# Kernel tuning notes

Measured on AMD Instinct MI355X. Metric: run time of the kernel, lower is better.

## Reference

```python
import jax, jax.numpy as jnp
import numpy as np

D_MODEL, D_K, D_V, H = 1024, 64, 64, 16
LN_EPS = 1e-5


def setup_inputs() -> dict:
    key = jax.random.key(0)
    ks = jax.random.split(key, 16)
    B, NQ, NK = 2, 1024, 1024
    queries = jax.random.normal(ks[0], (B, NQ, D_MODEL), dtype=jnp.float32)
    keys = jax.random.normal(ks[1], (B, NK, D_MODEL), dtype=jnp.float32)
    values = jax.random.normal(ks[2], (B, NK, D_MODEL), dtype=jnp.float32)
    attention_mask = jax.random.randint(ks[3], (B, H, NQ, NK), 0, 2).astype(jnp.bool_)
    attention_weights = jax.random.uniform(ks[4], (B, H, NQ, NK), dtype=jnp.float32)
    # Linear params, stored (in, out) so x @ W + b
    def xavier(k, shape):
        lim = float(np.sqrt(6.0 / (shape[0] + shape[1])))
        return jax.random.uniform(k, shape, jnp.float32, -lim, lim)
    Wq = xavier(ks[5], (D_MODEL, H * D_K)); bq = jnp.zeros((H * D_K,), jnp.float32)
    Wk = xavier(ks[6], (D_MODEL, H * D_K)); bk = jnp.zeros((H * D_K,), jnp.float32)
    Wv = xavier(ks[7], (D_MODEL, H * D_V)); bv = jnp.zeros((H * D_V,), jnp.float32)
    Wo = xavier(ks[8], (H * D_V, D_MODEL)); bo = jnp.zeros((D_MODEL,), jnp.float32)
    gamma = jnp.ones((D_MODEL,), jnp.float32)
    beta = jnp.zeros((D_MODEL,), jnp.float32)
    return dict(queries=queries, keys=keys, values=values,
                attention_mask=attention_mask, attention_weights=attention_weights,
                Wq=Wq, bq=bq, Wk=Wk, bk=bk, Wv=Wv, bv=bv, Wo=Wo, bo=bo,
                gamma=gamma, beta=beta)


def layer_norm(x, gamma, beta):
    mu = jnp.mean(x, axis=-1, keepdims=True)
    var = jnp.mean(jnp.square(x - mu), axis=-1, keepdims=True)
    return (x - mu) * jax.lax.rsqrt(var + LN_EPS) * gamma + beta


def reference(queries, keys, values, attention_mask, attention_weights,
              Wq, bq, Wk, bk, Wv, bv, Wo, bo, gamma, beta):
    B, NQ, _ = queries.shape
    NK = keys.shape[1]
    q = (queries @ Wq + bq).reshape(B, NQ, H, D_K).transpose(0, 2, 1, 3)  # b h nq dk
    k = (keys @ Wk + bk).reshape(B, NK, H, D_K).transpose(0, 2, 1, 3)    # b h nk dk
    v = (values @ Wv + bv).reshape(B, NK, H, D_V).transpose(0, 2, 1, 3)  # b h nk dv
    att = jnp.einsum('bhqd,bhkd->bhqk', q, k) / jnp.sqrt(jnp.float32(D_K))
    att = att * attention_weights
    att = jnp.where(attention_mask, -jnp.inf, att)
    att = jax.nn.softmax(att, axis=-1)  # dropout is identity in eval
    out = jnp.einsum('bhqk,bhkd->bhqd', att, v)
    out = out.transpose(0, 2, 1, 3).reshape(B, NQ, H * D_V)
    out = out @ Wo + bo
    # post-LN residual (identity_map_reordering=False)
    return layer_norm(queries + out, gamma, beta)
```

## Files before the change

kernel.cpp:

```cpp
#include <hip/hip_runtime.h>
#include <hip/hip_bf16.h>
#include <math.h>

#define B_   2
#define H_   16
#define NSEQ 1024
#define DM   1024
#define DKV  64
#define LNEPS 1e-5f

typedef __attribute__((ext_vector_type(8))) short s16x8;
typedef __attribute__((ext_vector_type(4))) float f32x4;
typedef __attribute__((ext_vector_type(4))) unsigned u32x4;

__device__ inline short f2bf(float f) {
    __hip_bfloat16 h = __float2bfloat16(f);
    return *reinterpret_cast<short*>(&h);
}

__global__ void detect_mask(const unsigned* __restrict__ mask_words, int* __restrict__ flag) {
    unsigned f = 0;
    for (int i = 0; i < 256; ++i) f |= (mask_words[i] > 1u) ? 1u : 0u;
    *flag = (int)f;
}

__global__ __launch_bounds__(256) void cast_bf16(const float* __restrict__ in,
                                                 short* __restrict__ out, int n) {
    int i = (blockIdx.x * 256 + threadIdx.x) * 8;
    if (i >= n) return;
    f32x4 a = *(const f32x4*)(in + i);
    f32x4 b = *(const f32x4*)(in + i + 4);
    s16x8 o;
    o[0]=f2bf(a[0]); o[1]=f2bf(a[1]); o[2]=f2bf(a[2]); o[3]=f2bf(a[3]);
    o[4]=f2bf(b[0]); o[5]=f2bf(b[1]); o[6]=f2bf(b[2]); o[7]=f2bf(b[3]);
    *(s16x8*)(out + i) = o;
}

__global__ __launch_bounds__(256) void castT_bf16(const float* __restrict__ W,
                                                  short* __restrict__ Wt) {
    __shared__ float tl[32][33];
    const int k0 = blockIdx.y * 32, n0 = blockIdx.x * 32;
    const int r = threadIdx.x >> 3, c4 = (threadIdx.x & 7) * 4;
    *(float4*)&tl[r][c4] = *(const float4*)(W + (size_t)(k0 + r) * DM + n0 + c4);
    __syncthreads();
    unsigned u0 = (unsigned short)f2bf(tl[c4+0][r]) | ((unsigned)(unsigned short)f2bf(tl[c4+1][r]) << 16);
    unsigned u1 = (unsigned short)f2bf(tl[c4+2][r]) | ((unsigned)(unsigned short)f2bf(tl[c4+3][r]) << 16);
    uint2 pk; pk.x = u0; pk.y = u1;
    *(uint2*)(Wt + (size_t)(n0 + r) * DM + k0 + c4) = pk;
}

__global__ __launch_bounds__(256) void gemm_bf16(
    const short* __restrict__ A, const short* __restrict__ Wt,
    const float* __restrict__ bias, const float* __restrict__ resid,
    void* __restrict__ outp, int mode)
{
    const int t  = threadIdx.x;
    const int wv = t >> 6, l = t & 63, lg = l >> 4, li = l & 15;
    const int wr = wv >> 1, wc = wv & 1;
    const int c0 = blockIdx.x * 64, m0 = blockIdx.y * 64;

    __shared__ short Asl[64 * 64];
    __shared__ short Bsl[64 * 64];

    f32x4 acc[2][2] = {};

    const int sr = t >> 2, scol = (t & 3) * 16;
    const int sw = (sr & 7) << 3;

    s16x8 a0 = *(const s16x8*)(A  + (size_t)(m0 + sr) * DM + scol);
    s16x8 a1 = *(const s16x8*)(A  + (size_t)(m0 + sr) * DM + scol + 8);
    s16x8 b0 = *(const s16x8*)(Wt + (size_t)(c0 + sr) * DM + scol);
    s16x8 b1 = *(const s16x8*)(Wt + (size_t)(c0 + sr) * DM + scol + 8);

    for (int k0 = 0; k0 < DM; k0 += 64) {
        __syncthreads();
        *(s16x8*)&Asl[sr * 64 + (scol ^ sw)]       = a0;
        *(s16x8*)&Asl[sr * 64 + ((scol + 8) ^ sw)] = a1;
        *(s16x8*)&Bsl[sr * 64 + (scol ^ sw)]       = b0;
        *(s16x8*)&Bsl[sr * 64 + ((scol + 8) ^ sw)] = b1;
        __syncthreads();
        if (k0 + 64 < DM) {
            a0 = *(const s16x8*)(A  + (size_t)(m0 + sr) * DM + k0 + 64 + scol);
            a1 = *(const s16x8*)(A  + (size_t)(m0 + sr) * DM + k0 + 64 + scol + 8);
            b0 = *(const s16x8*)(Wt + (size_t)(c0 + sr) * DM + k0 + 64 + scol);
            b1 = *(const s16x8*)(Wt + (size_t)(c0 + sr) * DM + k0 + 64 + scol + 8);
        }
        #pragma unroll
        for (int kh = 0; kh < 2; ++kh) {
            s16x8 af[2], bf[2];
            #pragma unroll
            for (int fi = 0; fi < 2; ++fi) {
                const int row = wr * 32 + fi * 16 + li;
                af[fi] = *(const s16x8*)&Asl[row * 64 + ((kh * 32 + lg * 8) ^ ((row & 7) << 3))];
            }
            #pragma unroll
            for (int fj = 0; fj < 2; ++fj) {
                const int row = wc * 32 + fj * 16 + li;
                bf[fj] = *(const s16x8*)&Bsl[row * 64 + ((kh * 32 + lg * 8) ^ ((row & 7) << 3))];
            }
            #pragma unroll
            for (int fi = 0; fi < 2; ++fi)
                #pragma unroll
                for (int fj = 0; fj < 2; ++fj)
                    acc[fi][fj] = __builtin_amdgcn_mfma_f32_16x16x32_bf16(af[fi], bf[fj], acc[fi][fj], 0, 0, 0);
        }
    }

    const int hh = c0 >> 6;
    #pragma unroll
    for (int fi = 0; fi < 2; ++fi) {
        #pragma unroll
        for (int j = 0; j < 4; ++j) {
            const int m = m0 + wr * 32 + fi * 16 + lg * 4 + j;
            const int bb = m >> 10, n = m & (NSEQ - 1);
            #pragma unroll
            for (int fj = 0; fj < 2; ++fj) {
                const int cc = wc * 32 + fj * 16 + li;
                const int c  = c0 + cc;
                float v = acc[fi][fj][j] + bias[c];
                if (mode == 1) {
                    ((short*)outp)[(((size_t)(bb * H_ + hh) * NSEQ) + n) * DKV + cc] = f2bf(v);
                } else if (mode == 2) {
                    ((short*)outp)[(((size_t)(bb * H_ + hh) * DKV) + cc) * NSEQ + n] = f2bf(v);
                } else {
                    float* of = (float*)outp;
                    of[(size_t)m * DM + c] = v + resid[(size_t)m * DM + c];
                }
            }
        }
    }
}


#define LOADC(kc_, kf_, w4_, mb_) do {                                                    \
    _Pragma("unroll") for (int dc = 0; dc < 2; ++dc)                                      \
      _Pragma("unroll") for (int nt = 0; nt < 4; ++nt)                                    \
        kf_[dc*4+nt] = *(const s16x8*)(Kp + (size_t)((kc_) + nt*16 + li) * DKV + dc*32 + lg*8); \
    _Pragma("unroll") for (int nt = 0; nt < 4; ++nt) {                                    \
        w4_[nt] = *(const f32x4*)(wrow + (kc_) + nt*16 + lg*4);                           \
        mb_[nt] = *(const unsigned*)(Mb + moff + (kc_) + nt*16 + lg*4);                   \
    }                                                                                     \
} while (0)

#define PROCESS(kc_, kf_, w4_, mb_) do {                                                  \
    f32x4 sc[4] = {};                                                                     \
    _Pragma("unroll") for (int dc = 0; dc < 2; ++dc)                                      \
      _Pragma("unroll") for (int nt = 0; nt < 4; ++nt)                                    \
        sc[nt] = __builtin_amdgcn_mfma_f32_16x16x32_bf16(kf_[dc*4+nt], qa[dc], sc[nt], 0, 0, 0); \
    s16x8 vf[8];                                                                          \
    _Pragma("unroll") for (int kch = 0; kch < 2; ++kch)                                   \
      _Pragma("unroll") for (int dt = 0; dt < 4; ++dt)                                    \
        vf[kch*4+dt] = *(const s16x8*)(Vp + (size_t)(dt*16 + li) * NSEQ + (kc_) + kch*32 + lg*8); \
    float sv[16]; float cmax = -1e30f;                                                    \
    _Pragma("unroll") for (int nt = 0; nt < 4; ++nt) {                                    \
      unsigned mm[4];                                                                     \
      if (mmode) { unsigned u = mb_[nt];                                                  \
        mm[0] = u & 0xffu; mm[1] = (u >> 8) & 0xffu; mm[2] = (u >> 16) & 0xffu; mm[3] = u >> 24; } \
      else { u32x4 mi = *(const u32x4*)(Mi + moff + (kc_) + nt*16 + lg*4);                \
        mm[0] = mi[0]; mm[1] = mi[1]; mm[2] = mi[2]; mm[3] = mi[3]; }                     \
      _Pragma("unroll") for (int r = 0; r < 4; ++r) {                                     \
        float s = sc[nt][r] * 0.125f * w4_[nt][r];                                        \
        s = mm[r] ? -1e30f : s;                                                           \
        sv[nt*4+r] = s; cmax = fmaxf(cmax, s); } }                                        \
    cmax = fmaxf(cmax, __shfl_xor(cmax, 16));                                             \
    cmax = fmaxf(cmax, __shfl_xor(cmax, 32));                                             \
    const float mnew = fmaxf(m_run, cmax);                                                \
    const float factor = __expf(m_run - mnew);                                            \
    m_run = mnew;                                                                         \
    float csum = 0.f;                                                                     \
    _Pragma("unroll") for (int nt = 0; nt < 4; ++nt) {                                    \
      float p0 = __expf(sv[nt*4+0] - mnew), p1 = __expf(sv[nt*4+1] - mnew);               \
      float p2 = __expf(sv[nt*4+2] - mnew), p3 = __expf(sv[nt*4+3] - mnew);               \
      csum += p0 + p1 + p2 + p3;                                                          \
      unsigned u0 = (unsigned short)f2bf(p0) | ((unsigned)(unsigned short)f2bf(p1) << 16);\
      unsigned u1 = (unsigned short)f2bf(p2) | ((unsigned)(unsigned short)f2bf(p3) << 16);\
      uint2 pk; pk.x = u0; pk.y = u1;                                                     \
      *(uint2*)&Plds[wv][li][nt*16 + lg*4] = pk; }                                        \
    csum += __shfl_xor(csum, 16); csum += __shfl_xor(csum, 32);                           \
    l_run = l_run * factor + csum;                                                        \
    float ffac[4];                                                                        \
    _Pragma("unroll") for (int r = 0; r < 4; ++r) ffac[r] = __shfl(factor, lg*4 + r);     \
    _Pragma("unroll") for (int dt = 0; dt < 4; ++dt)                                      \
      _Pragma("unroll") for (int r = 0; r < 4; ++r) oacc[dt][r] *= ffac[r];               \
    _Pragma("unroll") for (int kch = 0; kch < 2; ++kch) {                                 \
      s16x8 pa = *(const s16x8*)&Plds[wv][li][kch*32 + lg*8];                             \
      _Pragma("unroll") for (int dt = 0; dt < 4; ++dt)                                    \
        oacc[dt] = __builtin_amdgcn_mfma_f32_16x16x32_bf16(pa, vf[kch*4+dt], oacc[dt], 0, 0, 0); } \
} while (0)

__global__ __launch_bounds__(256) void attn_mfma(
    const short* __restrict__ Qb, const short* __restrict__ Kb, const short* __restrict__ Vt,
    const void* __restrict__ mask, const float* __restrict__ wgt,
    const int* __restrict__ flagp, short* __restrict__ O)
{
    const int t  = threadIdx.x;
    const int wv = t >> 6;
    const int l  = t & 63;
    const int lg = l >> 4;
    const int li = l & 15;
    const int qt = blockIdx.x;
    const int h  = blockIdx.y, b = blockIdx.z;
    const size_t bh = (size_t)b * H_ + h;
    const int qrow = qt*64 + wv*16 + li;

    __shared__ short Plds[4][16][80];

    const short* Qp = Qb + (bh * NSEQ + qt*64 + wv*16) * DKV;
    const short* Kp = Kb + bh * NSEQ * DKV;
    const short* Vp = Vt + bh * DKV * NSEQ;
    const float* wrow = wgt + (bh * NSEQ + qrow) * NSEQ;
    const size_t moff = (bh * NSEQ + qrow) * NSEQ;
    const int mmode = *flagp;
    const unsigned* Mi = (const unsigned*)mask;
    const unsigned char* Mb = (const unsigned char*)mask;

    s16x8 qa[2];
    qa[0] = *(const s16x8*)(Qp + (size_t)li * DKV + lg*8);
    qa[1] = *(const s16x8*)(Qp + (size_t)li * DKV + 32 + lg*8);

    float m_run = -1e30f, l_run = 0.f;
    f32x4 oacc[4] = {};

    s16x8 kfa[8], kfb[8];
    f32x4 w4a[4], w4b[4];
    unsigned mba[4], mbb[4];

    LOADC(0, kfa, w4a, mba);
    for (int kc = 0; kc < NSEQ; kc += 128) {
        LOADC(kc + 64, kfb, w4b, mbb);
        PROCESS(kc, kfa, w4a, mba);
        if (kc + 128 < NSEQ) LOADC(kc + 128, kfa, w4a, mba);
        PROCESS(kc + 64, kfb, w4b, mbb);
    }

    float rinv[4];
    #pragma unroll
    for (int r = 0; r < 4; ++r) rinv[r] = 1.0f / __shfl(l_run, lg*4 + r);
    #pragma unroll
    for (int dt = 0; dt < 4; ++dt)
        #pragma unroll
        for (int r = 0; r < 4; ++r)
            O[((size_t)b*NSEQ + qt*64 + wv*16 + lg*4 + r) * DM + h*DKV + dt*16 + li]
                = f2bf(oacc[dt][r] * rinv[r]);
}

__global__ __launch_bounds__(256) void ln_kernel(
    const float* __restrict__ Y, const float* __restrict__ gamma,
    const float* __restrict__ beta, float* __restrict__ out)
{
    const int row = blockIdx.x;
    const int t = threadIdx.x;
    const float* y = Y + (size_t)row * DM;
    float4 x = *(const float4*)(y + t*4);
    __shared__ float red[4];
    float s = x.x + x.y + x.z + x.w;
    #pragma unroll
    for (int off = 32; off > 0; off >>= 1) s += __shfl_xor(s, off);
    if ((t & 63) == 0) red[t >> 6] = s;
    __syncthreads();
    float mean = (red[0]+red[1]+red[2]+red[3]) * (1.0f/DM);
    float d0 = x.x-mean, d1 = x.y-mean, d2 = x.z-mean, d3 = x.w-mean;
    float sq = d0*d0 + d1*d1 + d2*d2 + d3*d3;
    __syncthreads();
    #pragma unroll
    for (int off = 32; off > 0; off >>= 1) sq += __shfl_xor(sq, off);
    if ((t & 63) == 0) red[t >> 6] = sq;
    __syncthreads();
    float var = (red[0]+red[1]+red[2]+red[3]) * (1.0f/DM);
    float rstd = rsqrtf(var + LNEPS);
    int c = t * 4;
    float4 g  = *(const float4*)(gamma + c);
    float4 bb = *(const float4*)(beta + c);
    float4 o;
    o.x = d0*rstd*g.x + bb.x;
    o.y = d1*rstd*g.y + bb.y;
    o.z = d2*rstd*g.z + bb.z;
    o.w = d3*rstd*g.w + bb.w;
    *(float4*)(out + (size_t)row*DM + c) = o;
}

extern "C" void kernel_launch(void* const* d_in, const int* in_sizes, int n_in,
                              void* d_out, int out_size, void* d_ws, size_t ws_size,
                              hipStream_t stream)
{
    const float* queries = (const float*)d_in[0];
    const float* keys    = (const float*)d_in[1];
    const float* values  = (const float*)d_in[2];
    const void*  mask    = d_in[3];
    const float* wgt     = (const float*)d_in[4];
    const float* Wq = (const float*)d_in[5];  const float* bq = (const float*)d_in[6];
    const float* Wk = (const float*)d_in[7];  const float* bk = (const float*)d_in[8];
    const float* Wv = (const float*)d_in[9];  const float* bv = (const float*)d_in[10];
    const float* Wo = (const float*)d_in[11]; const float* bo = (const float*)d_in[12];
    const float* gamma = (const float*)d_in[13]; const float* beta = (const float*)d_in[14];
    float* out = (float*)d_out;

    const size_t SZ = (size_t)B_ * NSEQ * DM;
    const size_t WSZ = (size_t)DM * DM;

    char* ws = (char*)d_ws;
    int* flag  = (int*)ws;
    short* Qa  = (short*)(ws + 256);
    short* Ka  = Qa + SZ;
    short* Va  = Ka + SZ;
    short* Wtq = Va + SZ;
    short* Wtk = Wtq + WSZ;
    short* Wtv = Wtk + WSZ;
    short* Wto = Wtv + WSZ;
    short* Qh  = Wto + WSZ;
    short* Kh  = Qh + SZ;
    short* Vth = Kh + SZ;
    short* Ob  = Va;
    float* Yb  = (float*)Qa;

    detect_mask<<<1, 1, 0, stream>>>((const unsigned*)mask, flag);
    cast_bf16<<<dim3((int)(SZ/8/256)), 256, 0, stream>>>(queries, Qa, (int)SZ);
    cast_bf16<<<dim3((int)(SZ/8/256)), 256, 0, stream>>>(keys,    Ka, (int)SZ);
    cast_bf16<<<dim3((int)(SZ/8/256)), 256, 0, stream>>>(values,  Va, (int)SZ);
    castT_bf16<<<dim3(32, 32), 256, 0, stream>>>(Wq, Wtq);
    castT_bf16<<<dim3(32, 32), 256, 0, stream>>>(Wk, Wtk);
    castT_bf16<<<dim3(32, 32), 256, 0, stream>>>(Wv, Wtv);
    castT_bf16<<<dim3(32, 32), 256, 0, stream>>>(Wo, Wto);

    gemm_bf16<<<dim3(16, 32), 256, 0, stream>>>(Qa, Wtq, bq, nullptr, Qh, 1);
    gemm_bf16<<<dim3(16, 32), 256, 0, stream>>>(Ka, Wtk, bk, nullptr, Kh, 1);
    gemm_bf16<<<dim3(16, 32), 256, 0, stream>>>(Va, Wtv, bv, nullptr, Vth, 2);

    attn_mfma<<<dim3(16, H_, B_), 256, 0, stream>>>(Qh, Kh, Vth, mask, wgt, flag, Ob);

    gemm_bf16<<<dim3(16, 32), 256, 0, stream>>>(Ob, Wto, bo, queries, Yb, 0);
    ln_kernel<<<dim3(B_*NSEQ), 256, 0, stream>>>(Yb, gamma, beta, out);
}
```

Measured before the change: 200.8 us.

## Split attention over key dimension with combine pass, batch cast launches

Splits the attention kernel four ways along the key sequence, so each block handles a quarter of the keys and writes partial outputs plus running max and sum. A new combine kernel merges the partials with log-sum-exp rescaling. This quadruples the attention grid to fill more compute units. It also merges the three input casts and four weight transposes into single launches. The split drops the old double-buffered prefetch of K, weights and mask, adds extra global traffic for the bf16 partials, and rounds the partial outputs to bf16 before the combine.

Result: faster. 193.6 us (-3.6%).

```diff
diff --git a/kernel.cpp b/kernel.cpp
--- a/kernel.cpp
+++ b/kernel.cpp
@@ -7,6 +7,8 @@
 #define NSEQ 1024
 #define DM   1024
 #define DKV  64
+#define NSPLIT 4
+#define KPB  (NSEQ / NSPLIT)
 #define LNEPS 1e-5f
 
 typedef __attribute__((ext_vector_type(8))) short s16x8;
@@ -16,6 +18,10 @@
 __device__ inline short f2bf(float f) {
     __hip_bfloat16 h = __float2bfloat16(f);
     return *reinterpret_cast<short*>(&h);
+}
+__device__ inline float bf2f(short s) {
+    unsigned u = ((unsigned)(unsigned short)s) << 16;
+    return __uint_as_float(u);
 }
 
 __global__ void detect_mask(const unsigned* __restrict__ mask_words, int* __restrict__ flag) {
@@ -24,8 +30,11 @@
     *flag = (int)f;
 }
 
-__global__ __launch_bounds__(256) void cast_bf16(const float* __restrict__ in,
-                                                 short* __restrict__ out, int n) {
+__global__ __launch_bounds__(256) void cast3_bf16(
+    const float* __restrict__ q, const float* __restrict__ k, const float* __restrict__ v,
+    short* __restrict__ qo, short* __restrict__ ko, short* __restrict__ vo, int n) {
+    const float* in = blockIdx.y == 0 ? q : (blockIdx.y == 1 ? k : v);
+    short* out      = blockIdx.y == 0 ? qo : (blockIdx.y == 1 ? ko : vo);
     int i = (blockIdx.x * 256 + threadIdx.x) * 8;
     if (i >= n) return;
     f32x4 a = *(const f32x4*)(in + i);
@@ -36,8 +45,13 @@
     *(s16x8*)(out + i) = o;
 }
 
-__global__ __launch_bounds__(256) void castT_bf16(const float* __restrict__ W,
-                                                  short* __restrict__ Wt) {
+__global__ __launch_bounds__(256) void castT4_bf16(
+    const float* __restrict__ w0, const float* __restrict__ w1,
+    const float* __restrict__ w2, const float* __restrict__ w3,
+    short* __restrict__ t0, short* __restrict__ t1,
+    short* __restrict__ t2, short* __restrict__ t3) {
+    const float* W = blockIdx.z == 0 ? w0 : (blockIdx.z == 1 ? w1 : (blockIdx.z == 2 ? w2 : w3));
+    short* Wt      = blockIdx.z == 0 ? t0 : (blockIdx.z == 1 ? t1 : (blockIdx.z == 2 ? t2 : t3));
     __shared__ float tl[32][33];
     const int k0 = blockIdx.y * 32, n0 = blockIdx.x * 32;
     const int r = threadIdx.x >> 3, c4 = (threadIdx.x & 7) * 4;
@@ -131,77 +145,23 @@
     }
 }
 
-
-#define LOADC(kc_, kf_, w4_, mb_) do {                                                    \
-    _Pragma("unroll") for (int dc = 0; dc < 2; ++dc)                                      \
-      _Pragma("unroll") for (int nt = 0; nt < 4; ++nt)                                    \
-        kf_[dc*4+nt] = *(const s16x8*)(Kp + (size_t)((kc_) + nt*16 + li) * DKV + dc*32 + lg*8); \
-    _Pragma("unroll") for (int nt = 0; nt < 4; ++nt) {                                    \
-        w4_[nt] = *(const f32x4*)(wrow + (kc_) + nt*16 + lg*4);                           \
-        mb_[nt] = *(const unsigned*)(Mb + moff + (kc_) + nt*16 + lg*4);                   \
-    }                                                                                     \
-} while (0)
-
-#define PROCESS(kc_, kf_, w4_, mb_) do {                                                  \
-    f32x4 sc[4] = {};                                                                     \
-    _Pragma("unroll") for (int dc = 0; dc < 2; ++dc)                                      \
-      _Pragma("unroll") for (int nt = 0; nt < 4; ++nt)                                    \
-        sc[nt] = __builtin_amdgcn_mfma_f32_16x16x32_bf16(kf_[dc*4+nt], qa[dc], sc[nt], 0, 0, 0); \
-    s16x8 vf[8];                                                                          \
-    _Pragma("unroll") for (int kch = 0; kch < 2; ++kch)                                   \
-      _Pragma("unroll") for (int dt = 0; dt < 4; ++dt)                                    \
-        vf[kch*4+dt] = *(const s16x8*)(Vp + (size_t)(dt*16 + li) * NSEQ + (kc_) + kch*32 + lg*8); \
-    float sv[16]; float cmax = -1e30f;                                                    \
-    _Pragma("unroll") for (int nt = 0; nt < 4; ++nt) {                                    \
-      unsigned mm[4];                                                                     \
-      if (mmode) { unsigned u = mb_[nt];                                                  \
-        mm[0] = u & 0xffu; mm[1] = (u >> 8) & 0xffu; mm[2] = (u >> 16) & 0xffu; mm[3] = u >> 24; } \
-      else { u32x4 mi = *(const u32x4*)(Mi + moff + (kc_) + nt*16 + lg*4);                \
-        mm[0] = mi[0]; mm[1] = mi[1]; mm[2] = mi[2]; mm[3] = mi[3]; }                     \
-      _Pragma("unroll") for (int r = 0; r < 4; ++r) {                                     \
-        float s = sc[nt][r] * 0.125f * w4_[nt][r];                                        \
-        s = mm[r] ? -1e30f : s;                                                           \
-        sv[nt*4+r] = s; cmax = fmaxf(cmax, s); } }                                        \
-    cmax = fmaxf(cmax, __shfl_xor(cmax, 16));                                             \
-    cmax = fmaxf(cmax, __shfl_xor(cmax, 32));                                             \
-    const float mnew = fmaxf(m_run, cmax);                                                \
-    const float factor = __expf(m_run - mnew);                                            \
-    m_run = mnew;                                                                         \
-    float csum = 0.f;                                                                     \
-    _Pragma("unroll") for (int nt = 0; nt < 4; ++nt) {                                    \
-      float p0 = __expf(sv[nt*4+0] - mnew), p1 = __expf(sv[nt*4+1] - mnew);               \
-      float p2 = __expf(sv[nt*4+2] - mnew), p3 = __expf(sv[nt*4+3] - mnew);               \
-      csum += p0 + p1 + p2 + p3;                                                          \
-      unsigned u0 = (unsigned short)f2bf(p0) | ((unsigned)(unsigned short)f2bf(p1) << 16);\
-      unsigned u1 = (unsigned short)f2bf(p2) | ((unsigned)(unsigned short)f2bf(p3) << 16);\
-      uint2 pk; pk.x = u0; pk.y = u1;                                                     \
-      *(uint2*)&Plds[wv][li][nt*16 + lg*4] = pk; }                                        \
-    csum += __shfl_xor(csum, 16); csum += __shfl_xor(csum, 32);                           \
-    l_run = l_run * factor + csum;                                                        \
-    float ffac[4];                                                                        \
-    _Pragma("unroll") for (int r = 0; r < 4; ++r) ffac[r] = __shfl(factor, lg*4 + r);     \
-    _Pragma("unroll") for (int dt = 0; dt < 4; ++dt)                                      \
-      _Pragma("unroll") for (int r = 0; r < 4; ++r) oacc[dt][r] *= ffac[r];               \
-    _Pragma("unroll") for (int kch = 0; kch < 2; ++kch) {                                 \
-      s16x8 pa = *(const s16x8*)&Plds[wv][li][kch*32 + lg*8];                             \
-      _Pragma("unroll") for (int dt = 0; dt < 4; ++dt)                                    \
-        oacc[dt] = __builtin_amdgcn_mfma_f32_16x16x32_bf16(pa, vf[kch*4+dt], oacc[dt], 0, 0, 0); } \
-} while (0)
-
-__global__ __launch_bounds__(256) void attn_mfma(
+__global__ __launch_bounds__(256) void attn_split(
     const short* __restrict__ Qb, const short* __restrict__ Kb, const short* __restrict__ Vt,
     const void* __restrict__ mask, const float* __restrict__ wgt,
-    const int* __restrict__ flagp, short* __restrict__ O)
+    const int* __restrict__ flagp, short* __restrict__ Opart,
+    float* __restrict__ mpart, float* __restrict__ lpart)
 {
     const int t  = threadIdx.x;
     const int wv = t >> 6;
     const int l  = t & 63;
     const int lg = l >> 4;
     const int li = l & 15;
-    const int qt = blockIdx.x;
+    const int qt = blockIdx.x >> 2;
+    const int sp = blockIdx.x & (NSPLIT-1);
     const int h  = blockIdx.y, b = blockIdx.z;
     const size_t bh = (size_t)b * H_ + h;
     const int qrow = qt*64 + wv*16 + li;
+    const int kbase = sp * KPB;
 
     __shared__ short Plds[4][16][80];
 
@@ -221,27 +181,123 @@
     float m_run = -1e30f, l_run = 0.f;
     f32x4 oacc[4] = {};
 
-    s16x8 kfa[8], kfb[8];
-    f32x4 w4a[4], w4b[4];
-    unsigned mba[4], mbb[4];
-
-    LOADC(0, kfa, w4a, mba);
-    for (int kc = 0; kc < NSEQ; kc += 128) {
-        LOADC(kc + 64, kfb, w4b, mbb);
-        PROCESS(kc, kfa, w4a, mba);
-        if (kc + 128 < NSEQ) LOADC(kc + 128, kfa, w4a, mba);
-        PROCESS(kc + 64, kfb, w4b, mbb);
-    }
-
-    float rinv[4];
-    #pragma unroll
-    for (int r = 0; r < 4; ++r) rinv[r] = 1.0f / __shfl(l_run, lg*4 + r);
+    for (int kc = kbase; kc < kbase + KPB; kc += 64) {
+        f32x4 sc[4] = {};
+        #pragma unroll
+        for (int dc = 0; dc < 2; ++dc)
+            #pragma unroll
+            for (int nt = 0; nt < 4; ++nt) {
+                s16x8 kb = *(const s16x8*)(Kp + (size_t)(kc + nt*16 + li) * DKV + dc*32 + lg*8);
+                sc[nt] = __builtin_amdgcn_mfma_f32_16x16x32_bf16(kb, qa[dc], sc[nt], 0, 0, 0);
+            }
+
+        s16x8 vf[8];
+        #pragma unroll
+        for (int kch = 0; kch < 2; ++kch)
+            #pragma unroll
+            for (int dt = 0; dt < 4; ++dt)
+                vf[kch*4+dt] = *(const s16x8*)(Vp + (size_t)(dt*16 + li) * NSEQ + kc + kch*32 + lg*8);
+
+        float sv[16];
+        float cmax = -1e30f;
+        #pragma unroll
+        for (int nt = 0; nt < 4; ++nt) {
+            const int k4 = kc + nt*16 + lg*4;
+            f32x4 w4 = *(const f32x4*)(wrow + k4);
+            unsigned mm[4];
+            if (mmode) {
+                unsigned u = *(const unsigned*)(Mb + moff + k4);
+                mm[0] = u & 0xffu; mm[1] = (u >> 8) & 0xffu;
+                mm[2] = (u >> 16) & 0xffu; mm[3] = u >> 24;
+            } else {
+                u32x4 mi = *(const u32x4*)(Mi + moff + k4);
+                mm[0] = mi[0]; mm[1] = mi[1]; mm[2] = mi[2]; mm[3] = mi[3];
+            }
+            #pragma unroll
+            for (int r = 0; r < 4; ++r) {
+                float s = sc[nt][r] * 0.125f * w4[r];
+                s = mm[r] ? -1e30f : s;
+                sv[nt*4 + r] = s;
+                cmax = fmaxf(cmax, s);
+            }
+        }
+        cmax = fmaxf(cmax, __shfl_xor(cmax, 16));
+        cmax = fmaxf(cmax, __shfl_xor(cmax, 32));
+        const float mnew = fmaxf(m_run, cmax);
+        const float factor = __expf(m_run - mnew);
+        m_run = mnew;
+
+        float csum = 0.f;
+        #pragma unroll
+        for (int nt = 0; nt < 4; ++nt) {
+            float p0 = __expf(sv[nt*4+0] - mnew), p1 = __expf(sv[nt*4+1] - mnew);
+            float p2 = __expf(sv[nt*4+2] - mnew), p3 = __expf(sv[nt*4+3] - mnew);
+            csum += p0 + p1 + p2 + p3;
+            unsigned u0 = (unsigned short)f2bf(p0) | ((unsigned)(unsigned short)f2bf(p1) << 16);
+            unsigned u1 = (unsigned short)f2bf(p2) | ((unsigned)(unsigned short)f2bf(p3) << 16);
+            uint2 pk; pk.x = u0; pk.y = u1;
+            *(uint2*)&Plds[wv][li][nt*16 + lg*4] = pk;
+        }
+        csum += __shfl_xor(csum, 16);
+        csum += __shfl_xor(csum, 32);
+        l_run = l_run * factor + csum;
+
+        float ffac[4];
+        #pragma unroll
+        for (int r = 0; r < 4; ++r) ffac[r] = __shfl(factor, lg*4 + r);
+        #pragma unroll
+        for (int dt = 0; dt < 4; ++dt)
+            #pragma unroll
+            for (int r = 0; r < 4; ++r)
+                oacc[dt][r] *= ffac[r];
+
+        #pragma unroll
+        for (int kch = 0; kch < 2; ++kch) {
+            s16x8 pa = *(const s16x8*)&Plds[wv][li][kch*32 + lg*8];
+            #pragma unroll
+            for (int dt = 0; dt < 4; ++dt)
+                oacc[dt] = __builtin_amdgcn_mfma_f32_16x16x32_bf16(pa, vf[kch*4+dt], oacc[dt], 0, 0, 0);
+        }
+    }
+
+    const size_t SBH = (size_t)B_ * H_ * NSEQ;
+    if (lg == 0) {
+        mpart[(size_t)sp * SBH + bh * NSEQ + qrow] = m_run;
+        lpart[(size_t)sp * SBH + bh * NSEQ + qrow] = l_run;
+    }
     #pragma unroll
     for (int dt = 0; dt < 4; ++dt)
         #pragma unroll
         for (int r = 0; r < 4; ++r)
-            O[((size_t)b*NSEQ + qt*64 + wv*16 + lg*4 + r) * DM + h*DKV + dt*16 + li]
-                = f2bf(oacc[dt][r] * rinv[r]);
+            Opart[((size_t)sp * SBH + bh * NSEQ + qt*64 + wv*16 + lg*4 + r) * DKV + dt*16 + li]
+                = f2bf(oacc[dt][r]);
+}
+
+__global__ __launch_bounds__(256) void attn_combine(
+    const short* __restrict__ Opart, const float* __restrict__ mpart,
+    const float* __restrict__ lpart, short* __restrict__ Ob)
+{
+    const size_t SBH = (size_t)B_ * H_ * NSEQ;
+    const int R = blockIdx.x * 4 + (threadIdx.x >> 6);
+    const int d = threadIdx.x & 63;
+    const int bh = R >> 10, n = R & (NSEQ - 1);
+    const int b = bh >> 4, h = bh & (H_ - 1);
+
+    float ms[NSPLIT];
+    float mstar = -1e30f;
+    #pragma unroll
+    for (int s = 0; s < NSPLIT; ++s) {
+        ms[s] = mpart[(size_t)s * SBH + R];
+        mstar = fmaxf(mstar, ms[s]);
+    }
+    float lstar = 0.f, acc = 0.f;
+    #pragma unroll
+    for (int s = 0; s < NSPLIT; ++s) {
+        float w = __expf(ms[s] - mstar);
+        lstar += w * lpart[(size_t)s * SBH + R];
+        acc   += w * bf2f(Opart[((size_t)s * SBH + R) * DKV + d]);
+    }
+    Ob[((size_t)b * NSEQ + n) * DM + h * DKV + d] = f2bf(acc / lstar);
 }
 
 __global__ __launch_bounds__(256) void ln_kernel(
@@ -295,8 +351,9 @@
     const float* gamma = (const float*)d_in[13]; const float* beta = (const float*)d_in[14];
     float* out = (float*)d_out;
 
-    const size_t SZ = (size_t)B_ * NSEQ * DM;
+    const size_t SZ  = (size_t)B_ * NSEQ * DM;
     const size_t WSZ = (size_t)DM * DM;
+    const size_t SBH = (size_t)B_ * H_ * NSEQ;
 
     char* ws = (char*)d_ws;
     int* flag  = (int*)ws;
@@ -310,23 +367,23 @@
     short* Qh  = Wto + WSZ;
     short* Kh  = Qh + SZ;
     short* Vth = Kh + SZ;
+    short* Opart = Vth + SZ;
+    float* mpart = (float*)(Opart + (size_t)NSPLIT * SBH * DKV);
+    float* lpart = mpart + (size_t)NSPLIT * SBH;
     short* Ob  = Va;
     float* Yb  = (float*)Qa;
 
     detect_mask<<<1, 1, 0, stream>>>((const unsigned*)mask, flag);
-    cast_bf16<<<dim3((int)(SZ/8/256)), 256, 0, stream>>>(queries, Qa, (int)SZ);
-    cast_bf16<<<dim3((int)(SZ/8/256)), 256, 0, stream>>>(keys,    Ka, (int)SZ);
-    cast_bf16<<<dim3((int)(SZ/8/256)), 256, 0, stream>>>(values,  Va, (int)SZ);
-    castT_bf16<<<dim3(32, 32), 256, 0, stream>>>(Wq, Wtq);
-    castT_bf16<<<dim3(32, 32), 256, 0, stream>>>(Wk, Wtk);
-    castT_bf16<<<dim3(32, 32), 256, 0, stream>>>(Wv, Wtv);
-    castT_bf16<<<dim3(32, 32), 256, 0, stream>>>(Wo, Wto);
+    cast3_bf16<<<dim3((int)(SZ/8/256), 3), 256, 0, stream>>>(queries, keys, values, Qa, Ka, Va, (int)SZ);
+    castT4_bf16<<<dim3(32, 32, 4), 256, 0, stream>>>(Wq, Wk, Wv, Wo, Wtq, Wtk, Wtv, Wto);
 
     gemm_bf16<<<dim3(16, 32), 256, 0, stream>>>(Qa, Wtq, bq, nullptr, Qh, 1);
     gemm_bf16<<<dim3(16, 32), 256, 0, stream>>>(Ka, Wtk, bk, nullptr, Kh, 1);
     gemm_bf16<<<dim3(16, 32), 256, 0, stream>>>(Va, Wtv, bv, nullptr, Vth, 2);
 
-    attn_mfma<<<dim3(16, H_, B_), 256, 0, stream>>>(Qh, Kh, Vth, mask, wgt, flag, Ob);
+    attn_split<<<dim3(16 * NSPLIT, H_, B_), 256, 0, stream>>>(Qh, Kh, Vth, mask, wgt, flag,
+                                                              Opart, mpart, lpart);
+    attn_combine<<<dim3((int)(SBH / 4)), 256, 0, stream>>>(Opart, mpart, lpart, Ob);
 
     gemm_bf16<<<dim3(16, 32), 256, 0, stream>>>(Ob, Wto, bo, queries, Yb, 0);
     ln_kernel<<<dim3(B_*NSEQ), 256, 0, stream>>>(Yb, gamma, beta, out);
```
